# Kernel optimization log

Hardware: AMD Instinct MI355X
Metric: run time of the kernel (lower is better)

Reference implementation:

```python
import jax, jax.numpy as jnp
import numpy as np

CLS_NUM = 2
SCALE = 8.0
NO_OBJ_SCALE = 1.0
EPS = 1e-7


def setup_inputs() -> dict:
    key = jax.random.key(0)
    k1, k2, k3, k4, k5, k6 = jax.random.split(key, 6)
    B, C, H, W, N = 8, CLS_NUM, 512, 512, 160
    predict = jax.random.normal(k1, (B, C, H, W), dtype=jnp.float32)
    b = jax.random.randint(k2, (N,), 0, B).astype(jnp.float32)
    c = jax.random.randint(k3, (N,), 0, C).astype(jnp.float32)
    cxy = jax.random.uniform(k4, (N, 2), minval=0.0, maxval=H * SCALE)
    wh = jax.random.uniform(k5, (N, 2), minval=64.0, maxval=256.0)
    ang = jax.random.uniform(k6, (N, 1), minval=-np.pi, maxval=np.pi)
    targets = jnp.concatenate([b[:, None], c[:, None], cxy, wh, ang], axis=1).astype(jnp.float32)
    return {"predict": predict, "targets": targets}


def _forward(predict, targets):
    B, C, H, W = predict.shape
    pred = jnp.transpose(predict, (0, 2, 3, 1))          # [B,H,W,C]
    conf_all = jax.nn.sigmoid(pred)
    heatmap = jnp.max(conf_all, axis=-1)                 # [B,H,W]

    bid = targets[:, 0].astype(jnp.int32)                # [N] batch ids
    cid = targets[:, 1].astype(jnp.int32)                # [N] class ids
    cx = targets[:, 2] / SCALE
    cy = targets[:, 3] / SCALE
    w = targets[:, 4] / SCALE
    h = targets[:, 5] / SCALE
    ang = targets[:, 6]
    cos, sin = jnp.cos(ang), jnp.sin(ang)
    # rotate box center into the rotated frame (same math as render_map)
    x = cx * cos + cy * sin
    y = -cx * sin + cy * cos
    x3, x4 = x - h / 2, x + h / 2
    y3, y4 = y - w / 2, y + w / 2
    x1, x2 = x3 - 0.5, x4 + 0.5
    y1, y2 = y3 - 0.5, y4 + 0.5

    gx = jnp.arange(W, dtype=jnp.float32)[None, :] + 0.5  # [1,W] -> broadcasts to [H,W]
    gy = jnp.arange(H, dtype=jnp.float32)[:, None] + 0.5  # [H,1]
    vx = cos[:, None, None] * gx + sin[:, None, None] * gy   # [N,H,W]
    vy = -sin[:, None, None] * gx + cos[:, None, None] * gy  # [N,H,W]

    def box_mask(lo_x, hi_x, lo_y, hi_y):
        return ((lo_x[:, None, None] <= vx) & (vx <= hi_x[:, None, None]) &
                (lo_y[:, None, None] <= vy) & (vy <= hi_y[:, None, None]))

    inner = box_mask(x3, x4, y3, y4)  # obj region, [N,H,W]
    outer = box_mask(x1, x2, y1, y2)  # expanded region (clears noobj)

    loss = jnp.float32(0.0)
    for cls in range(CLS_NUM):
        sel = (cid == cls)[:, None, None]
        obj_cnt = jax.ops.segment_sum((inner & sel).astype(jnp.float32), bid, num_segments=B)
        out_cnt = jax.ops.segment_sum((outer & sel).astype(jnp.float32), bid, num_segments=B)
        obj_mask = obj_cnt > 0            # [B,H,W]
        noobj_mask = out_cnt <= 0         # starts at 1, zeroed inside any expanded box
        conf_c = jnp.clip(conf_all[..., cls], EPS, 1.0 - EPS)
        n_obj = jnp.sum(obj_mask)
        n_noobj = jnp.sum(noobj_mask)
        # BCE with target 1 on obj cells, target 0 on noobj cells (tconf == obj mask)
        loss_obj = -jnp.sum(jnp.where(obj_mask, jnp.log(conf_c), 0.0)) / jnp.maximum(n_obj, 1)
        loss_noobj = -jnp.sum(jnp.where(noobj_mask, jnp.log(1.0 - conf_c), 0.0)) / jnp.maximum(n_noobj, 1)
        loss = loss + jnp.where(n_obj > 0, loss_obj + NO_OBJ_SCALE * loss_noobj, 0.0)
    return loss, heatmap


def reference(predict, targets):
    return _forward(predict, targets)
```

## Files before the change

kernel.cpp:

```cpp
#include <hip/hip_runtime.h>
#include <math.h>

#define CLS 2
#define BATCH 8
#define HH 512
#define WW 512
#define INV_SCALE 0.125f
#define LOGEPS -16.118095651f

#define NB 512
#define TSTRIDE 192


__global__ __launch_bounds__(256) void heatmap_prep(
    const float* __restrict__ targets, int nT, double* __restrict__ gsum,
    int* __restrict__ gcnt, int* __restrict__ bcnt, float* __restrict__ tdat)
{
    __shared__ int s_b[BATCH];
    const int t = threadIdx.x;
    if (t < BATCH) s_b[t] = 0;
    for (int q = t; q < 4 * NB; q += 256) { gsum[q] = 0.0; gcnt[q] = 0; }
    __syncthreads();
    if (t < nT) {
        const float* tp = targets + t * 7;
        const int b = (int)tp[0];
        const float cs = cosf(tp[6]), sn = sinf(tp[6]);
        const float cx = tp[2] * INV_SCALE, cy = tp[3] * INV_SCALE;
        const float w_ = tp[4] * INV_SCALE, h_ = tp[5] * INV_SCALE;
        const float x = cx * cs + cy * sn;
        const float y = -cx * sn + cy * cs;
        const int slot = atomicAdd(&s_b[b], 1);
        float* tbp = tdat + b * (7 * TSTRIDE);
        tbp[0 * TSTRIDE + slot] = cs;
        tbp[1 * TSTRIDE + slot] = sn;
        tbp[2 * TSTRIDE + slot] = x - 0.5f * h_;
        tbp[3 * TSTRIDE + slot] = x + 0.5f * h_;
        tbp[4 * TSTRIDE + slot] = y - 0.5f * w_;
        tbp[5 * TSTRIDE + slot] = y + 0.5f * w_;
        ((int*)tbp)[6 * TSTRIDE + slot] = (int)tp[1];
    }
    __syncthreads();
    if (t < BATCH) bcnt[t] = s_b[t];
}

__global__ __launch_bounds__(256) void heatmap_main(
    const float* __restrict__ predict, float* __restrict__ out,
    double* __restrict__ gsum, int* __restrict__ gcnt,
    const int* __restrict__ bcnt, const float* __restrict__ tdat)
{
    const int wid = threadIdx.x >> 6;
    const int l   = threadIdx.x & 63;
    const int sidx = blockIdx.x * 4 + wid;
    const int blockPix = sidx * 256;
    const int b  = blockPix >> 18;
    const int i  = (blockPix >> 9) & (HH - 1);
    const int j0 = blockPix & (WW - 1);
    const float gy = (float)i + 0.5f;

    const int j = j0 + 4 * l;
    const float gxb = (float)j + 0.5f;

    const int nb = bcnt[b];
    const float* tbp = tdat + b * (7 * TSTRIDE);

    int objm[4] = {0, 0, 0, 0}, outm[4] = {0, 0, 0, 0};

    for (int base = 0; base < nb; base += 64) {
        const int t = base + l;
        float cs = 0.f, sn = 0.f, x3 = 0.f, x4 = 0.f, y3 = 0.f, y4 = 0.f;
        int cid = 0;
        bool acc = false;
        if (t < nb) {
            cs = tbp[0 * TSTRIDE + t]; sn = tbp[1 * TSTRIDE + t];
            x3 = tbp[2 * TSTRIDE + t]; x4 = tbp[3 * TSTRIDE + t];
            y3 = tbp[4 * TSTRIDE + t]; y4 = tbp[5 * TSTRIDE + t];
            cid = ((const int*)tbp)[6 * TSTRIDE + t];
            const float gxl = (float)j0 + 0.5f, gxh = (float)j0 + 255.5f;
            const float a1 = cs * gxl + sn * gy, a2 = cs * gxh + sn * gy;
            const float b1 = -sn * gxl + cs * gy, b2 = -sn * gxh + cs * gy;
            const float vxlo = fminf(a1, a2), vxhi = fmaxf(a1, a2);
            const float vylo = fminf(b1, b2), vyhi = fmaxf(b1, b2);
            const float M = 0.51f;
            acc = (vxhi >= x3 - M) & (vxlo <= x4 + M) &
                  (vyhi >= y3 - M) & (vylo <= y4 + M);
        }
        unsigned long long bal = __ballot(acc);
        while (bal) {
            const int n = __builtin_ctzll(bal);
            bal &= bal - 1;
            const float ccs = __shfl(cs, n), csn = __shfl(sn, n);
            const float cx3 = __shfl(x3, n), cx4 = __shfl(x4, n);
            const float cy3 = __shfl(y3, n), cy4 = __shfl(y4, n);
            const int cbit = 1 << __shfl(cid, n);
            float vx = ccs * gxb + csn * gy;
            float vy = -csn * gxb + ccs * gy;
            #pragma unroll
            for (int k = 0; k < 4; ++k) {
                const bool in_  = (cx3 <= vx) & (vx <= cx4) &
                                  (cy3 <= vy) & (vy <= cy4);
                const bool out_ = (cx3 - 0.5f <= vx) & (vx <= cx4 + 0.5f) &
                                  (cy3 - 0.5f <= vy) & (vy <= cy4 + 0.5f);
                if (in_)  objm[k] |= cbit;
                if (out_) outm[k] |= cbit;
                vx += ccs; vy -= csn;
            }
        }
    }

    const int pbase = (b * CLS * HH + i) * WW + j;
    const float4 P0 = *(const float4*)(predict + pbase);
    const float4 P1 = *(const float4*)(predict + pbase + HH * WW);

    float so0 = 0.f, so1 = 0.f, sq0 = 0.f, sq1 = 0.f;
    int c_obj0 = 0, c_obj1 = 0, c_no0 = 0, c_no1 = 0;
    float hm[4];
    #pragma unroll
    for (int k = 0; k < 4; ++k) {
        const float p0 = (&P0.x)[k], p1 = (&P1.x)[k];
        const float t0 = __expf(p0), t1 = __expf(p1);
        const float l0n = -__logf(1.0f + t0);
        const float l1n = -__logf(1.0f + t1);
        const float lc0 = fmaxf(p0 + l0n, LOGEPS);
        const float lc1 = fmaxf(p1 + l1n, LOGEPS);
        const float l0c = fmaxf(l0n, LOGEPS);
        const float l1c = fmaxf(l1n, LOGEPS);
        const float tm = fmaxf(t0, t1);
        hm[k] = tm * __builtin_amdgcn_rcpf(1.0f + tm);
        const int om = objm[k], um = outm[k];
        if (om & 1) { so0 += lc0; ++c_obj0; }
        if (om & 2) { so1 += lc1; ++c_obj1; }
        if (!(um & 1)) { sq0 += l0c; ++c_no0; }
        if (!(um & 2)) { sq1 += l1c; ++c_no1; }
    }

    float* ho = out + 1 + (b * HH + i) * WW + j;
    ho[0] = hm[0]; ho[1] = hm[1]; ho[2] = hm[2]; ho[3] = hm[3];

    const unsigned long long anyobj =
        __ballot((objm[0] | objm[1] | objm[2] | objm[3]) != 0);
    int pc = (c_no0 & 0xffff) | (c_no1 << 16);
    #pragma unroll
    for (int off = 32; off >= 1; off >>= 1) {
        sq0 += __shfl_down(sq0, off);
        sq1 += __shfl_down(sq1, off);
        pc  += __shfl_down(pc, off);
    }
    int po = 0;
    if (anyobj) {
        po = (c_obj0 & 0xffff) | (c_obj1 << 16);
        #pragma unroll
        for (int off = 32; off >= 1; off >>= 1) {
            so0 += __shfl_down(so0, off);
            so1 += __shfl_down(so1, off);
            po  += __shfl_down(po, off);
        }
    }
    if (l == 0) {
        const int bkt = sidx & (NB - 1);
        atomicAdd(&gsum[2 * NB + bkt], (double)sq0);
        atomicAdd(&gsum[3 * NB + bkt], (double)sq1);
        atomicAdd(&gcnt[2 * NB + bkt], pc & 0xffff);
        atomicAdd(&gcnt[3 * NB + bkt], pc >> 16);
        if (anyobj) {
            const int o0 = po & 0xffff, o1 = po >> 16;
            if (o0) { atomicAdd(&gsum[0 * NB + bkt], (double)so0);
                      atomicAdd(&gcnt[0 * NB + bkt], o0); }
            if (o1) { atomicAdd(&gsum[1 * NB + bkt], (double)so1);
                      atomicAdd(&gcnt[1 * NB + bkt], o1); }
        }
    }
}

__global__ __launch_bounds__(512) void heatmap_finalize(
    const double* __restrict__ gsum, const int* __restrict__ gcnt,
    float* __restrict__ out)
{
    const int t = threadIdx.x;
    double f[4]; int c[4];
    #pragma unroll
    for (int q = 0; q < 4; ++q) { f[q] = gsum[q * NB + t]; c[q] = gcnt[q * NB + t]; }

    #pragma unroll
    for (int off = 32; off >= 1; off >>= 1) {
        #pragma unroll
        for (int q = 0; q < 4; ++q) {
            f[q] += __shfl_down(f[q], off);
            c[q] += __shfl_down(c[q], off);
        }
    }

    __shared__ double sf[8][4];
    __shared__ int    si[8][4];
    const int wv = t >> 6, ln = t & 63;
    if (ln == 0) {
        #pragma unroll
        for (int q = 0; q < 4; ++q) { sf[wv][q] = f[q]; si[wv][q] = c[q]; }
    }
    __syncthreads();
    if (t == 0) {
        double F[4] = {0, 0, 0, 0}; int C[4] = {0, 0, 0, 0};
        for (int w = 0; w < 8; ++w)
            #pragma unroll
            for (int q = 0; q < 4; ++q) { F[q] += sf[w][q]; C[q] += si[w][q]; }
        float loss = 0.0f;
        #pragma unroll
        for (int cls = 0; cls < CLS; ++cls) {
            const int no = C[cls];
            const int nn = C[2 + cls];
            if (no > 0) {
                const float lo  = -(float)F[cls]     / (float)(no > 1 ? no : 1);
                const float ln_ = -(float)F[2 + cls] / (float)(nn > 1 ? nn : 1);
                loss += lo + ln_;
            }
        }
        out[0] = loss;
    }
}

extern "C" void kernel_launch(void* const* d_in, const int* in_sizes, int n_in,
                              void* d_out, int out_size, void* d_ws, size_t ws_size,
                              hipStream_t stream) {
    const float* predict = (const float*)d_in[0];
    const float* targets = (const float*)d_in[1];
    const int nT = in_sizes[1] / 7;
    float* out = (float*)d_out;
    char* ws = (char*)d_ws;
    double* gsum = (double*)ws;
    int* gcnt = (int*)(ws + 16384);
    int* bcnt = (int*)(ws + 24576);
    float* tdat = (float*)(ws + 24608);

    heatmap_prep<<<1, 256, 0, stream>>>(targets, nT, gsum, gcnt, bcnt, tdat);
    const int nstrips = BATCH * HH * WW / 256;
    heatmap_main<<<nstrips / 4, 256, 0, stream>>>(predict, out, gsum, gcnt,
                                                  bcnt, tdat);
    heatmap_finalize<<<1, 512, 0, stream>>>(gsum, gcnt, out);
}
```

Before: 80.77 us.

## Fold target preprocessing into main kernel and replace atomics with per-block partials

```diff
diff --git a/kernel.cpp b/kernel.cpp
--- a/kernel.cpp
+++ b/kernel.cpp
@@ -8,91 +8,80 @@
 #define INV_SCALE 0.125f
 #define LOGEPS -16.118095651f
 
-#define NB 512
-#define TSTRIDE 192
-
-
-__global__ __launch_bounds__(256) void heatmap_prep(
-    const float* __restrict__ targets, int nT, double* __restrict__ gsum,
-    int* __restrict__ gcnt, int* __restrict__ bcnt, float* __restrict__ tdat)
+#define MAXT 256
+#define NBLK 2048
+
+
+__global__ __launch_bounds__(256) void heatmap_main(
+    const float* __restrict__ predict, const float* __restrict__ targets,
+    int nT, float* __restrict__ out,
+    double* __restrict__ gsumd, int* __restrict__ gcnti)
 {
-    __shared__ int s_b[BATCH];
-    const int t = threadIdx.x;
-    if (t < BATCH) s_b[t] = 0;
-    for (int q = t; q < 4 * NB; q += 256) { gsum[q] = 0.0; gcnt[q] = 0; }
-    __syncthreads();
-    if (t < nT) {
-        const float* tp = targets + t * 7;
-        const int b = (int)tp[0];
-        const float cs = cosf(tp[6]), sn = sinf(tp[6]);
-        const float cx = tp[2] * INV_SCALE, cy = tp[3] * INV_SCALE;
-        const float w_ = tp[4] * INV_SCALE, h_ = tp[5] * INV_SCALE;
-        const float x = cx * cs + cy * sn;
-        const float y = -cx * sn + cy * cs;
-        const int slot = atomicAdd(&s_b[b], 1);
-        float* tbp = tdat + b * (7 * TSTRIDE);
-        tbp[0 * TSTRIDE + slot] = cs;
-        tbp[1 * TSTRIDE + slot] = sn;
-        tbp[2 * TSTRIDE + slot] = x - 0.5f * h_;
-        tbp[3 * TSTRIDE + slot] = x + 0.5f * h_;
-        tbp[4 * TSTRIDE + slot] = y - 0.5f * w_;
-        tbp[5 * TSTRIDE + slot] = y + 0.5f * w_;
-        ((int*)tbp)[6 * TSTRIDE + slot] = (int)tp[1];
-    }
-    __syncthreads();
-    if (t < BATCH) bcnt[t] = s_b[t];
-}
-
-__global__ __launch_bounds__(256) void heatmap_main(
-    const float* __restrict__ predict, float* __restrict__ out,
-    double* __restrict__ gsum, int* __restrict__ gcnt,
-    const int* __restrict__ bcnt, const float* __restrict__ tdat)
-{
-    const int wid = threadIdx.x >> 6;
-    const int l   = threadIdx.x & 63;
-    const int sidx = blockIdx.x * 4 + wid;
-    const int blockPix = sidx * 256;
-    const int b  = blockPix >> 18;
-    const int i  = (blockPix >> 9) & (HH - 1);
-    const int j0 = blockPix & (WW - 1);
+    __shared__ float s_cs[MAXT], s_sn[MAXT], s_x3[MAXT], s_x4[MAXT],
+                     s_y3[MAXT], s_y4[MAXT];
+    __shared__ int s_cid[MAXT];
+    __shared__ int s_nb;
+    __shared__ double s_bs[4][4];
+    __shared__ int s_bc[4][2];
+
+    const int tid = threadIdx.x;
+    const int blockPix = blockIdx.x << 10;
+    const int b = blockPix >> 18;
+
+    if (tid == 0) s_nb = 0;
+    __syncthreads();
+    for (int t0 = tid; t0 < nT; t0 += 256) {
+        const float* tp = targets + t0 * 7;
+        if ((int)tp[0] == b) {
+            const float cs = cosf(tp[6]), sn = sinf(tp[6]);
+            const float cx = tp[2] * INV_SCALE, cy = tp[3] * INV_SCALE;
+            const float w_ = tp[4] * INV_SCALE, h_ = tp[5] * INV_SCALE;
+            const float x =  cx * cs + cy * sn;
+            const float y = -cx * sn + cy * cs;
+            const int slot = atomicAdd(&s_nb, 1);
+            s_cs[slot] = cs; s_sn[slot] = sn;
+            s_x3[slot] = x - 0.5f * h_; s_x4[slot] = x + 0.5f * h_;
+            s_y3[slot] = y - 0.5f * w_; s_y4[slot] = y + 0.5f * w_;
+            s_cid[slot] = (int)tp[1];
+        }
+    }
+    __syncthreads();
+    const int nb = s_nb;
+
+    const int wid = tid >> 6;
+    const int l   = tid & 63;
+    const int spix = blockPix + (wid << 8);
+    const int i  = (spix >> 9) & (HH - 1);
+    const int j0 = spix & (WW - 1);
     const float gy = (float)i + 0.5f;
-
     const int j = j0 + 4 * l;
     const float gxb = (float)j + 0.5f;
 
-    const int nb = bcnt[b];
-    const float* tbp = tdat + b * (7 * TSTRIDE);
-
     int objm[4] = {0, 0, 0, 0}, outm[4] = {0, 0, 0, 0};
 
     for (int base = 0; base < nb; base += 64) {
         const int t = base + l;
-        float cs = 0.f, sn = 0.f, x3 = 0.f, x4 = 0.f, y3 = 0.f, y4 = 0.f;
-        int cid = 0;
         bool acc = false;
         if (t < nb) {
-            cs = tbp[0 * TSTRIDE + t]; sn = tbp[1 * TSTRIDE + t];
-            x3 = tbp[2 * TSTRIDE + t]; x4 = tbp[3 * TSTRIDE + t];
-            y3 = tbp[4 * TSTRIDE + t]; y4 = tbp[5 * TSTRIDE + t];
-            cid = ((const int*)tbp)[6 * TSTRIDE + t];
+            const float cs = s_cs[t], sn = s_sn[t];
             const float gxl = (float)j0 + 0.5f, gxh = (float)j0 + 255.5f;
             const float a1 = cs * gxl + sn * gy, a2 = cs * gxh + sn * gy;
             const float b1 = -sn * gxl + cs * gy, b2 = -sn * gxh + cs * gy;
             const float vxlo = fminf(a1, a2), vxhi = fmaxf(a1, a2);
             const float vylo = fminf(b1, b2), vyhi = fmaxf(b1, b2);
             const float M = 0.51f;
-            acc = (vxhi >= x3 - M) & (vxlo <= x4 + M) &
-                  (vyhi >= y3 - M) & (vylo <= y4 + M);
+            acc = (vxhi >= s_x3[t] - M) & (vxlo <= s_x4[t] + M) &
+                  (vyhi >= s_y3[t] - M) & (vylo <= s_y4[t] + M);
         }
         unsigned long long bal = __ballot(acc);
         while (bal) {
-            const int n = __builtin_ctzll(bal);
+            const int n = base + __builtin_ctzll(bal);
             bal &= bal - 1;
-            const float ccs = __shfl(cs, n), csn = __shfl(sn, n);
-            const float cx3 = __shfl(x3, n), cx4 = __shfl(x4, n);
-            const float cy3 = __shfl(y3, n), cy4 = __shfl(y4, n);
-            const int cbit = 1 << __shfl(cid, n);
-            float vx = ccs * gxb + csn * gy;
+            const float ccs = s_cs[n], csn = s_sn[n];
+            const float cx3 = s_x3[n], cx4 = s_x4[n];
+            const float cy3 = s_y3[n], cy4 = s_y4[n];
+            const int cbit = 1 << s_cid[n];
+            float vx =  ccs * gxb + csn * gy;
             float vy = -csn * gxb + ccs * gy;
             #pragma unroll
             for (int k = 0; k < 4; ++k) {
@@ -156,63 +145,71 @@
         }
     }
     if (l == 0) {
-        const int bkt = sidx & (NB - 1);
-        atomicAdd(&gsum[2 * NB + bkt], (double)sq0);
-        atomicAdd(&gsum[3 * NB + bkt], (double)sq1);
-        atomicAdd(&gcnt[2 * NB + bkt], pc & 0xffff);
-        atomicAdd(&gcnt[3 * NB + bkt], pc >> 16);
-        if (anyobj) {
-            const int o0 = po & 0xffff, o1 = po >> 16;
-            if (o0) { atomicAdd(&gsum[0 * NB + bkt], (double)so0);
-                      atomicAdd(&gcnt[0 * NB + bkt], o0); }
-            if (o1) { atomicAdd(&gsum[1 * NB + bkt], (double)so1);
-                      atomicAdd(&gcnt[1 * NB + bkt], o1); }
-        }
+        s_bs[wid][0] = (double)so0; s_bs[wid][1] = (double)so1;
+        s_bs[wid][2] = (double)sq0; s_bs[wid][3] = (double)sq1;
+        s_bc[wid][0] = po;          s_bc[wid][1] = pc;
+    }
+    __syncthreads();
+    if (tid == 0) {
+        double o0 = 0, o1 = 0, q0 = 0, q1 = 0;
+        int P = 0, Q = 0;
+        #pragma unroll
+        for (int w = 0; w < 4; ++w) {
+            o0 += s_bs[w][0]; o1 += s_bs[w][1];
+            q0 += s_bs[w][2]; q1 += s_bs[w][3];
+            P  += s_bc[w][0]; Q  += s_bc[w][1];
+        }
+        const int blk = blockIdx.x;
+        gsumd[0 * NBLK + blk] = o0; gsumd[1 * NBLK + blk] = o1;
+        gsumd[2 * NBLK + blk] = q0; gsumd[3 * NBLK + blk] = q1;
+        gcnti[0 * NBLK + blk] = P;  gcnti[1 * NBLK + blk] = Q;
     }
 }
 
 __global__ __launch_bounds__(512) void heatmap_finalize(
-    const double* __restrict__ gsum, const int* __restrict__ gcnt,
+    const double* __restrict__ gsumd, const int* __restrict__ gcnti,
     float* __restrict__ out)
 {
     const int t = threadIdx.x;
-    double f[4]; int c[4];
-    #pragma unroll
-    for (int q = 0; q < 4; ++q) { f[q] = gsum[q * NB + t]; c[q] = gcnt[q * NB + t]; }
-
+    double f[4] = {0, 0, 0, 0};
+    int co0 = 0, co1 = 0, cn0 = 0, cn1 = 0;
+    for (int blk = t; blk < NBLK; blk += 512) {
+        #pragma unroll
+        for (int q = 0; q < 4; ++q) f[q] += gsumd[q * NBLK + blk];
+        const int p = gcnti[0 * NBLK + blk];
+        const int q2 = gcnti[1 * NBLK + blk];
+        co0 += p & 0xffff;  co1 += p >> 16;
+        cn0 += q2 & 0xffff; cn1 += q2 >> 16;
+    }
     #pragma unroll
     for (int off = 32; off >= 1; off >>= 1) {
         #pragma unroll
-        for (int q = 0; q < 4; ++q) {
-            f[q] += __shfl_down(f[q], off);
-            c[q] += __shfl_down(c[q], off);
-        }
+        for (int q = 0; q < 4; ++q) f[q] += __shfl_down(f[q], off);
+        co0 += __shfl_down(co0, off); co1 += __shfl_down(co1, off);
+        cn0 += __shfl_down(cn0, off); cn1 += __shfl_down(cn1, off);
     }
 
     __shared__ double sf[8][4];
-    __shared__ int    si[8][4];
+    __shared__ int    sc[8][4];
     const int wv = t >> 6, ln = t & 63;
     if (ln == 0) {
         #pragma unroll
-        for (int q = 0; q < 4; ++q) { sf[wv][q] = f[q]; si[wv][q] = c[q]; }
+        for (int q = 0; q < 4; ++q) sf[wv][q] = f[q];
+        sc[wv][0] = co0; sc[wv][1] = co1; sc[wv][2] = cn0; sc[wv][3] = cn1;
     }
     __syncthreads();
     if (t == 0) {
         double F[4] = {0, 0, 0, 0}; int C[4] = {0, 0, 0, 0};
         for (int w = 0; w < 8; ++w)
             #pragma unroll
-            for (int q = 0; q < 4; ++q) { F[q] += sf[w][q]; C[q] += si[w][q]; }
+            for (int q = 0; q < 4; ++q) { F[q] += sf[w][q]; C[q] += sc[w][q]; }
         float loss = 0.0f;
-        #pragma unroll
-        for (int cls = 0; cls < CLS; ++cls) {
-            const int no = C[cls];
-            const int nn = C[2 + cls];
-            if (no > 0) {
-                const float lo  = -(float)F[cls]     / (float)(no > 1 ? no : 1);
-                const float ln_ = -(float)F[2 + cls] / (float)(nn > 1 ? nn : 1);
-                loss += lo + ln_;
-            }
-        }
+        if (C[0] > 0)
+            loss += -(float)F[0] / (float)C[0]
+                    - (float)F[2] / (float)(C[2] > 0 ? C[2] : 1);
+        if (C[1] > 0)
+            loss += -(float)F[1] / (float)C[1]
+                    - (float)F[3] / (float)(C[3] > 0 ? C[3] : 1);
         out[0] = loss;
     }
 }
@@ -225,14 +222,10 @@
     const int nT = in_sizes[1] / 7;
     float* out = (float*)d_out;
     char* ws = (char*)d_ws;
-    double* gsum = (double*)ws;
-    int* gcnt = (int*)(ws + 16384);
-    int* bcnt = (int*)(ws + 24576);
-    float* tdat = (float*)(ws + 24608);
-
-    heatmap_prep<<<1, 256, 0, stream>>>(targets, nT, gsum, gcnt, bcnt, tdat);
-    const int nstrips = BATCH * HH * WW / 256;
-    heatmap_main<<<nstrips / 4, 256, 0, stream>>>(predict, out, gsum, gcnt,
-                                                  bcnt, tdat);
-    heatmap_finalize<<<1, 512, 0, stream>>>(gsum, gcnt, out);
+    double* gsumd = (double*)ws;
+    int* gcnti = (int*)(ws + 65536);
+
+    heatmap_main<<<NBLK, 256, 0, stream>>>(predict, targets, nT, out,
+                                           gsumd, gcnti);
+    heatmap_finalize<<<1, 512, 0, stream>>>(gsumd, gcnti, out);
 }
```

Result: faster. 79.15 us (-2.0%).
